# Performance work log

Measured on AMD Instinct MI355X. Metric: run time of the kernel, lower is better.

The kernel has to match this reference:

```python
import jax, jax.numpy as jnp
import numpy as np
import math

V, D, L, H, F, S_MAX = 32000, 512, 4, 8, 2048, 1024
DK = D // H
EPS = 1e-6


def _ln(x, g, b):
    # torch: gamma*(x-mean)/(std+eps)+beta with unbiased=False std, eps added to std
    mean = jnp.mean(x, axis=-1, keepdims=True)
    std = jnp.sqrt(jnp.mean((x - mean) ** 2, axis=-1, keepdims=True))
    return g * (x - mean) / (std + EPS) + b


def _pos_encoding(seq_len, d_model):
    pos = jnp.arange(seq_len, dtype=jnp.float32)[:, None]
    div = jnp.exp(jnp.arange(0, d_model, 2, dtype=jnp.float32) * (-math.log(10000.0) / d_model))
    pe = jnp.zeros((seq_len, d_model), dtype=jnp.float32)
    pe = pe.at[:, 0::2].set(jnp.sin(pos * div))
    pe = pe.at[:, 1::2].set(jnp.cos(pos * div))
    return pe


def setup_inputs() -> dict:
    key = jax.random.key(0)
    ks = jax.random.split(key, 20)
    n = lambda k, shape, s=0.02: (jax.random.normal(k, shape, dtype=jnp.float32) * s)
    inp = {
        "input_tokens": jax.random.randint(ks[0], (4, 1024), 0, V, dtype=jnp.int64),
        "tok_emb": n(ks[1], (V, D)),
        "gamma1": jnp.ones((L, D), jnp.float32), "beta1": jnp.zeros((L, D), jnp.float32),
        "wq": n(ks[2], (L, D, D)), "bq": jnp.zeros((L, D), jnp.float32),
        "wk": n(ks[3], (L, D, D)), "bk": jnp.zeros((L, D), jnp.float32),
        "wv": n(ks[4], (L, D, D)), "bv": jnp.zeros((L, D), jnp.float32),
        "wo": n(ks[5], (L, D, D)), "bo": jnp.zeros((L, D), jnp.float32),
        "gamma2": jnp.ones((L, D), jnp.float32), "beta2": jnp.zeros((L, D), jnp.float32),
        "w1": n(ks[6], (L, D, F)), "b1": jnp.zeros((L, F), jnp.float32),
        "w2": n(ks[7], (L, F, D)), "b2": jnp.zeros((L, D), jnp.float32),
        "gamma_f": jnp.ones((D,), jnp.float32), "beta_f": jnp.zeros((D,), jnp.float32),
        "w_out": n(ks[8], (D, V)), "b_out": jnp.zeros((V,), jnp.float32),
    }
    return inp


def reference(input_tokens, tok_emb, gamma1, beta1, wq, bq, wk, bk, wv, bv, wo, bo,
              gamma2, beta2, w1, b1, w2, b2, gamma_f, beta_f, w_out, b_out):
    B, S = input_tokens.shape
    # embedding * sqrt(d_model) + sinusoidal PE (dropout = identity in eval)
    x = tok_emb[input_tokens] * jnp.float32(math.sqrt(D)) + _pos_encoding(S, D)[None]
    causal = jnp.tril(jnp.ones((S, S), dtype=bool))[None, None]  # [1,1,S,S]
    scale = jnp.float32(1.0 / math.sqrt(DK))

    def block(x, p):
        g1, be1, Wq, Bq, Wk, Bk, Wv, Bv, Wo, Bo, g2, be2, W1, B1, W2, B2 = p
        h = _ln(x, g1, be1)
        q = (h @ Wq + Bq).reshape(B, S, H, DK).transpose(0, 2, 1, 3)
        k = (h @ Wk + Bk).reshape(B, S, H, DK).transpose(0, 2, 1, 3)
        v = (h @ Wv + Bv).reshape(B, S, H, DK).transpose(0, 2, 1, 3)
        scores = jnp.einsum('bhqd,bhkd->bhqk', q, k) * scale
        scores = jnp.where(causal, scores, jnp.float32(-1e9))  # masked_fill
        attn = jax.nn.softmax(scores, axis=-1)
        o = jnp.einsum('bhqk,bhkd->bhqd', attn, v)
        o = o.transpose(0, 2, 1, 3).reshape(B, S, D) @ Wo + Bo
        x = x + o
        h2 = _ln(x, g2, be2)
        ff = jax.nn.gelu(h2 @ W1 + B1, approximate=False) @ W2 + B2
        return x + ff, None

    params = (gamma1, beta1, wq, bq, wk, bk, wv, bv, wo, bo, gamma2, beta2, w1, b1, w2, b2)
    x, _ = jax.lax.scan(block, x, params)
    x = _ln(x, gamma_f, beta_f)
    logits = x @ w_out + b_out
    return logits
```

## Files before the change

### kernel.cpp

```cpp
#include <hip/hip_runtime.h>
#include <cstdint>
#include <cstddef>

typedef __attribute__((ext_vector_type(8))) short short8;
typedef __attribute__((ext_vector_type(4))) float f32x4;

#define DEV static __device__ __forceinline__

DEV short f2bf(float f) {
  unsigned u = __float_as_uint(f);
  u = (u + 0x7fffu + ((u >> 16) & 1u)) >> 16;
  return (short)u;
}

DEV void gload_lds16(const void* g, void* l) {
  __builtin_amdgcn_global_load_lds(
      (const __attribute__((address_space(1))) unsigned int*)(uintptr_t)g,
      (__attribute__((address_space(3))) unsigned int*)(uintptr_t)l,
      16, 0, 0);
}

DEV void transpose_tile32(const float* __restrict__ src, int sld,
                          short* __restrict__ dst, int dld,
                          int sr, int sc, int tid)
{
  __shared__ float tile[32][33];
  const int r = tid >> 5, c = tid & 31;
#pragma unroll
  for (int i = 0; i < 4; ++i)
    tile[r + 8 * i][c] = src[(size_t)(sr + r + 8 * i) * sld + sc + c];
  __syncthreads();
#pragma unroll
  for (int i = 0; i < 4; ++i)
    dst[(size_t)(sc + r + 8 * i) * dld + sr + c] = f2bf(tile[c][r + 8 * i]);
}

__global__ __launch_bounds__(256) void convert_all_k(
    const float* __restrict__ wq, const float* __restrict__ wk,
    const float* __restrict__ wv, const float* __restrict__ wo,
    const float* __restrict__ w1, const float* __restrict__ w2,
    const float* __restrict__ wout,
    const float* __restrict__ bq, const float* __restrict__ bk,
    const float* __restrict__ bv,
    short* __restrict__ wqkv_bt, short* __restrict__ wo_bt,
    short* __restrict__ w1_bt, short* __restrict__ w2_bt,
    short* __restrict__ wout_bt, float* __restrict__ bqkv)
{
  const int t = blockIdx.x, tid = threadIdx.x;
  if (t < 3072) {
    int layer = t / 768, rem = t % 768, mat = rem / 256, tt = rem % 256;
    int tr = tt / 16, tc = tt % 16;
    const float* src = (mat == 0 ? wq : mat == 1 ? wk : wv) + (size_t)layer * 262144;
    short* dst = wqkv_bt + (size_t)layer * 786432 + (size_t)mat * 262144;
    transpose_tile32(src, 512, dst, 512, tr * 32, tc * 32, tid);
  } else if (t < 4096) {
    int t2 = t - 3072;
    int layer = t2 / 256, tt = t2 % 256, tr = tt / 16, tc = tt % 16;
    transpose_tile32(wo + (size_t)layer * 262144, 512,
                     wo_bt + (size_t)layer * 262144, 512, tr * 32, tc * 32, tid);
  } else if (t < 8192) {
    int t2 = t - 4096;
    int layer = t2 / 1024, tt = t2 % 1024, tr = tt / 64, tc = tt % 64;
    transpose_tile32(w1 + (size_t)layer * 1048576, 2048,
                     w1_bt + (size_t)layer * 1048576, 512, tr * 32, tc * 32, tid);
  } else if (t < 12288) {
    int t2 = t - 8192;
    int layer = t2 / 1024, tt = t2 % 1024, tr = tt / 16, tc = tt % 16;
    transpose_tile32(w2 + (size_t)layer * 1048576, 512,
                     w2_bt + (size_t)layer * 1048576, 2048, tr * 32, tc * 32, tid);
  } else if (t < 28288) {
    int t2 = t - 12288;
    int tr = t2 / 1000, tc = t2 % 1000;
    transpose_tile32(wout, 32000, wout_bt, 512, tr * 32, tc * 32, tid);
  } else {
    int idx = (t - 28288) * 256 + tid;
    int layer = idx / 1536, j = idx % 1536;
    float v = (j < 512) ? bq[layer * 512 + j]
            : (j < 1024) ? bk[layer * 512 + j - 512]
                         : bv[layer * 512 + j - 1024];
    bqkv[idx] = v;
  }
}

__global__ __launch_bounds__(256) void embed_k(
    const int* __restrict__ tok, const float* __restrict__ emb, float* __restrict__ x)
{
  int idx = blockIdx.x * 256 + threadIdx.x;
  int d = idx & 511, bs = idx >> 9, s = bs & 1023;
  int t = tok[bs];
  float dv = expf((float)(d & ~1) * (-9.210340371976184f / 512.f));
  float ang = (float)s * dv;
  float pe = (d & 1) ? cosf(ang) : sinf(ang);
  x[idx] = emb[(size_t)t * 512 + d] * 22.62741699796952f + pe;
}

__global__ __launch_bounds__(256) void layernorm_k(
    const float* __restrict__ x, const float* __restrict__ g,
    const float* __restrict__ b, short* __restrict__ out)
{
  const int row = blockIdx.x, tid = threadIdx.x;
  const float* xr = x + (size_t)row * 512;
  float v0 = xr[tid], v1 = xr[tid + 256];
  float s = v0 + v1;
  __shared__ float rs[4], rq[4];
#pragma unroll
  for (int o = 32; o > 0; o >>= 1) s += __shfl_down(s, o, 64);
  if ((tid & 63) == 0) rs[tid >> 6] = s;
  __syncthreads();
  float mean = (rs[0] + rs[1] + rs[2] + rs[3]) * (1.f / 512.f);
  float d0 = v0 - mean, d1 = v1 - mean;
  float q = d0 * d0 + d1 * d1;
#pragma unroll
  for (int o = 32; o > 0; o >>= 1) q += __shfl_down(q, o, 64);
  if ((tid & 63) == 0) rq[tid >> 6] = q;
  __syncthreads();
  float var = (rq[0] + rq[1] + rq[2] + rq[3]) * (1.f / 512.f);
  float inv = 1.f / (sqrtf(var) + 1e-6f);
  out[(size_t)row * 512 + tid]       = f2bf(g[tid] * d0 * inv + b[tid]);
  out[(size_t)row * 512 + tid + 256] = f2bf(g[tid + 256] * d1 * inv + b[tid + 256]);
}

template<bool GELU, bool RES, bool OUTBF16>
__global__ __launch_bounds__(256) void gemm_bt(
    const short* __restrict__ A, const short* __restrict__ Bt,
    const float* __restrict__ bias, const float* __restrict__ resid,
    void* __restrict__ out, int M, int N, int K)
{
  __shared__ __align__(16) short lA[128 * 32];
  __shared__ __align__(16) short lB[128 * 32];
  const int tid = threadIdx.x;
  const int lane = tid & 63;
  const int w = tid >> 6, wr = w >> 1, wc = w & 1;
  const int lr = lane & 15, quad = lane >> 4;
  const int m0 = blockIdx.y * 128, n0 = blockIdx.x * 128;

  f32x4 acc[4][4] = {};

  const int c1 = tid, c2 = tid + 256;
  const short* Ab = A + (size_t)m0 * K;
  const short* Bb = Bt + (size_t)n0 * K;

  for (int k0 = 0; k0 < K; k0 += 32) {
    gload_lds16(Ab + (size_t)(c1 >> 2) * K + k0 + (c1 & 3) * 8, lA + c1 * 8);
    gload_lds16(Ab + (size_t)(c2 >> 2) * K + k0 + (c2 & 3) * 8, lA + c2 * 8);
    gload_lds16(Bb + (size_t)(c1 >> 2) * K + k0 + (c1 & 3) * 8, lB + c1 * 8);
    gload_lds16(Bb + (size_t)(c2 >> 2) * K + k0 + (c2 & 3) * 8, lB + c2 * 8);
    __syncthreads();
    short8 af[4], bf[4];
#pragma unroll
    for (int mi = 0; mi < 4; ++mi)
      af[mi] = *(const short8*)&lA[(wr * 64 + mi * 16 + lr) * 32 + quad * 8];
#pragma unroll
    for (int ni = 0; ni < 4; ++ni)
      bf[ni] = *(const short8*)&lB[(wc * 64 + ni * 16 + lr) * 32 + quad * 8];
#pragma unroll
    for (int mi = 0; mi < 4; ++mi)
#pragma unroll
      for (int ni = 0; ni < 4; ++ni)
        acc[mi][ni] = __builtin_amdgcn_mfma_f32_16x16x32_bf16(af[mi], bf[ni], acc[mi][ni], 0, 0, 0);
    __syncthreads();
  }

#pragma unroll
  for (int mi = 0; mi < 4; ++mi) {
#pragma unroll
    for (int ni = 0; ni < 4; ++ni) {
      const int n = n0 + wc * 64 + ni * 16 + lr;
      const float bn = bias[n];
#pragma unroll
      for (int r = 0; r < 4; ++r) {
        const int m = m0 + wr * 64 + mi * 16 + quad * 4 + r;
        float v = acc[mi][ni][r] + bn;
        if (GELU) v = 0.5f * v * (1.f + erff(v * 0.7071067811865475f));
        if (RES) v += resid[(size_t)m * N + n];
        if (OUTBF16) ((short*)out)[(size_t)m * N + n] = f2bf(v);
        else         ((float*)out)[(size_t)m * N + n] = v;
      }
    }
  }
}

__global__ __launch_bounds__(256) void attn_k(
    const short* __restrict__ qkv, short* __restrict__ attn_out)
{
  const int bh = blockIdx.y, b = bh >> 3, h = bh & 7;
  const int q0 = blockIdx.x * 64;
  const int tid = threadIdx.x, lane = tid & 63, w = tid >> 6;
  const int lr = lane & 15, quad = lane >> 4;
  const int RS = 1536;

  const short* qb = qkv + (size_t)b * 1024 * RS + h * 64;
  const short* kb = qb + 512;
  const short* vb = qb + 1024;

  __shared__ __align__(16) short lK[32 * 64];
  __shared__ __align__(16) short lVt[64 * 32];
  __shared__ __align__(16) short lP[4][16 * 32];

  const int qrow = q0 + w * 16 + lr;
  const short8 aq0 = *(const short8*)(qb + (size_t)qrow * RS + quad * 8);
  const short8 aq1 = *(const short8*)(qb + (size_t)qrow * RS + 32 + quad * 8);

  f32x4 o[4] = {};
  float mrow[4] = {-1e30f, -1e30f, -1e30f, -1e30f};
  float lrow[4] = {0.f, 0.f, 0.f, 0.f};

  const int kend = q0 + 64;
  for (int kt = 0; kt < kend; kt += 32) {
    {
      int r = tid >> 3, c = (tid & 7) * 8;
      gload_lds16(kb + (size_t)(kt + r) * RS + c, lK + r * 64 + c);
      short8 vv = *(const short8*)(vb + (size_t)(kt + r) * RS + c);
#pragma unroll
      for (int j = 0; j < 8; ++j) lVt[(c + j) * 32 + r] = vv[j];
    }
    __syncthreads();

    f32x4 st[2];
#pragma unroll
    for (int t = 0; t < 2; ++t) {
      const short8 bk0 = *(const short8*)&lK[(t * 16 + lr) * 64 + quad * 8];
      const short8 bk1 = *(const short8*)&lK[(t * 16 + lr) * 64 + 32 + quad * 8];
      f32x4 z = {0.f, 0.f, 0.f, 0.f};
      z = __builtin_amdgcn_mfma_f32_16x16x32_bf16(aq0, bk0, z, 0, 0, 0);
      z = __builtin_amdgcn_mfma_f32_16x16x32_bf16(aq1, bk1, z, 0, 0, 0);
      st[t] = z;
    }
    float sc[2][4];
#pragma unroll
    for (int t = 0; t < 2; ++t)
#pragma unroll
      for (int r = 0; r < 4; ++r) {
        int qg = q0 + w * 16 + quad * 4 + r;
        int kg = kt + t * 16 + lr;
        sc[t][r] = (kg <= qg) ? st[t][r] * 0.125f : -1e30f;
      }
#pragma unroll
    for (int r = 0; r < 4; ++r) {
      float tm = fmaxf(sc[0][r], sc[1][r]);
#pragma unroll
      for (int off = 1; off < 16; off <<= 1) tm = fmaxf(tm, __shfl_xor(tm, off, 64));
      float mnew = fmaxf(mrow[r], tm);
      float alpha = __expf(mrow[r] - mnew);
      mrow[r] = mnew;
      float p0 = __expf(sc[0][r] - mnew);
      float p1 = __expf(sc[1][r] - mnew);
      lP[w][(quad * 4 + r) * 32 + lr]      = f2bf(p0);
      lP[w][(quad * 4 + r) * 32 + 16 + lr] = f2bf(p1);
      float ps = p0 + p1;
#pragma unroll
      for (int off = 1; off < 16; off <<= 1) ps += __shfl_xor(ps, off, 64);
      lrow[r] = lrow[r] * alpha + ps;
#pragma unroll
      for (int ni = 0; ni < 4; ++ni) o[ni][r] *= alpha;
    }
    const short8 pa = *(const short8*)&lP[w][lr * 32 + quad * 8];
#pragma unroll
    for (int ni = 0; ni < 4; ++ni) {
      const short8 bv = *(const short8*)&lVt[(ni * 16 + lr) * 32 + quad * 8];
      o[ni] = __builtin_amdgcn_mfma_f32_16x16x32_bf16(pa, bv, o[ni], 0, 0, 0);
    }
    __syncthreads();
  }

#pragma unroll
  for (int ni = 0; ni < 4; ++ni)
#pragma unroll
    for (int r = 0; r < 4; ++r) {
      int qg = q0 + w * 16 + quad * 4 + r;
      float val = o[ni][r] / lrow[r];
      attn_out[((size_t)(b * 1024 + qg)) * 512 + h * 64 + ni * 16 + lr] = f2bf(val);
    }
}

extern "C" void kernel_launch(void* const* d_in, const int* in_sizes, int n_in,
                              void* d_out, int out_size, void* d_ws, size_t ws_size,
                              hipStream_t stream)
{
  (void)in_sizes; (void)n_in; (void)out_size; (void)ws_size;
  const int*   tokens  = (const int*)d_in[0];
  const float* tok_emb = (const float*)d_in[1];
  const float* gamma1  = (const float*)d_in[2];
  const float* beta1   = (const float*)d_in[3];
  const float* wq = (const float*)d_in[4];
  const float* bq = (const float*)d_in[5];
  const float* wk = (const float*)d_in[6];
  const float* bk = (const float*)d_in[7];
  const float* wv = (const float*)d_in[8];
  const float* bv = (const float*)d_in[9];
  const float* wo = (const float*)d_in[10];
  const float* bo = (const float*)d_in[11];
  const float* gamma2 = (const float*)d_in[12];
  const float* beta2  = (const float*)d_in[13];
  const float* w1 = (const float*)d_in[14];
  const float* b1 = (const float*)d_in[15];
  const float* w2 = (const float*)d_in[16];
  const float* b2 = (const float*)d_in[17];
  const float* gamma_f = (const float*)d_in[18];
  const float* beta_f  = (const float*)d_in[19];
  const float* w_out   = (const float*)d_in[20];
  const float* b_out   = (const float*)d_in[21];

  char* ws = (char*)d_ws;
  size_t off = 0;
  auto alloc = [&](size_t bytes) -> void* {
    void* p = ws + off; off += (bytes + 255) & ~(size_t)255; return p;
  };
  short* wqkv_bt = (short*)alloc(4ull * 1536 * 512 * 2);
  short* wo_bt   = (short*)alloc(4ull * 512 * 512 * 2);
  short* w1_bt   = (short*)alloc(4ull * 2048 * 512 * 2);
  short* w2_bt   = (short*)alloc(4ull * 512 * 2048 * 2);
  short* wout_bt = (short*)alloc(32000ull * 512 * 2);
  float* bqkv    = (float*)alloc(4ull * 1536 * 4);
  float* x       = (float*)alloc(4096ull * 512 * 4);
  short* hbuf    = (short*)alloc(4096ull * 512 * 2);
  short* qkv     = (short*)alloc(4096ull * 1536 * 2);
  short* attnout = (short*)alloc(4096ull * 512 * 2);
  short* ffn1    = (short*)alloc(4096ull * 2048 * 2);
  short* xf      = (short*)alloc(4096ull * 512 * 2);

  convert_all_k<<<28312, 256, 0, stream>>>(wq, wk, wv, wo, w1, w2, w_out, bq, bk, bv,
                                           wqkv_bt, wo_bt, w1_bt, w2_bt, wout_bt, bqkv);
  embed_k<<<8192, 256, 0, stream>>>(tokens, tok_emb, x);
  for (int l = 0; l < 4; ++l) {
    layernorm_k<<<4096, 256, 0, stream>>>(x, gamma1 + l * 512, beta1 + l * 512, hbuf);
    gemm_bt<false, false, true><<<dim3(12, 32), 256, 0, stream>>>(
        hbuf, wqkv_bt + (size_t)l * 786432, bqkv + l * 1536, nullptr, qkv, 4096, 1536, 512);
    attn_k<<<dim3(16, 32), 256, 0, stream>>>(qkv, attnout);
    gemm_bt<false, true, false><<<dim3(4, 32), 256, 0, stream>>>(
        attnout, wo_bt + (size_t)l * 262144, bo + l * 512, x, x, 4096, 512, 512);
    layernorm_k<<<4096, 256, 0, stream>>>(x, gamma2 + l * 512, beta2 + l * 512, hbuf);
    gemm_bt<true, false, true><<<dim3(16, 32), 256, 0, stream>>>(
        hbuf, w1_bt + (size_t)l * 1048576, b1 + l * 2048, nullptr, ffn1, 4096, 2048, 512);
    gemm_bt<false, true, false><<<dim3(4, 32), 256, 0, stream>>>(
        ffn1, w2_bt + (size_t)l * 1048576, b2 + l * 512, x, x, 4096, 512, 2048);
  }
  layernorm_k<<<4096, 256, 0, stream>>>(x, gamma_f, beta_f, xf);
  gemm_bt<false, false, false><<<dim3(250, 32), 256, 0, stream>>>(
      xf, wout_bt, b_out, nullptr, d_out, 4096, 32000, 512);
}
```

Before: 1.555 ms.

## Swizzle GEMM LDS layout and use 64-row tiles for N=512 GEMMs

Applies an XOR swizzle to the global-to-LDS source addressing and the matching fragment reads in the GEMM, to reduce LDS bank conflicts on the short8 loads. Adds a gemm64_bt variant with 64x128 tiles and uses it for the output-projection and FFN2 GEMMs (N=512). This doubles the grid from 128 to 256 blocks so more of the GPU's compute units are occupied. The smaller tiles lower per-block data reuse, and each wave computes a narrower 64x32 sub-tile.

Measured after the change: 1.504 ms. -3.3%, faster.

```diff
diff --git a/kernel.cpp b/kernel.cpp
--- a/kernel.cpp
+++ b/kernel.cpp
@@ -18,6 +18,11 @@
       (const __attribute__((address_space(1))) unsigned int*)(uintptr_t)g,
       (__attribute__((address_space(3))) unsigned int*)(uintptr_t)l,
       16, 0, 0);
+}
+
+DEV size_t swz_src(int c, int K, int k0) {
+  int r = c >> 2;
+  return (size_t)r * K + k0 + (size_t)(((c ^ r) & 3) << 3);
 }
 
 DEV void transpose_tile32(const float* __restrict__ src, int sld,
@@ -139,20 +144,21 @@
   const int c1 = tid, c2 = tid + 256;
   const short* Ab = A + (size_t)m0 * K;
   const short* Bb = Bt + (size_t)n0 * K;
+  const int sl = ((quad ^ lr) & 3) << 3;
 
   for (int k0 = 0; k0 < K; k0 += 32) {
-    gload_lds16(Ab + (size_t)(c1 >> 2) * K + k0 + (c1 & 3) * 8, lA + c1 * 8);
-    gload_lds16(Ab + (size_t)(c2 >> 2) * K + k0 + (c2 & 3) * 8, lA + c2 * 8);
-    gload_lds16(Bb + (size_t)(c1 >> 2) * K + k0 + (c1 & 3) * 8, lB + c1 * 8);
-    gload_lds16(Bb + (size_t)(c2 >> 2) * K + k0 + (c2 & 3) * 8, lB + c2 * 8);
+    gload_lds16(Ab + swz_src(c1, K, k0), lA + c1 * 8);
+    gload_lds16(Ab + swz_src(c2, K, k0), lA + c2 * 8);
+    gload_lds16(Bb + swz_src(c1, K, k0), lB + c1 * 8);
+    gload_lds16(Bb + swz_src(c2, K, k0), lB + c2 * 8);
     __syncthreads();
     short8 af[4], bf[4];
 #pragma unroll
     for (int mi = 0; mi < 4; ++mi)
-      af[mi] = *(const short8*)&lA[(wr * 64 + mi * 16 + lr) * 32 + quad * 8];
+      af[mi] = *(const short8*)&lA[(wr * 64 + mi * 16 + lr) * 32 + sl];
 #pragma unroll
     for (int ni = 0; ni < 4; ++ni)
-      bf[ni] = *(const short8*)&lB[(wc * 64 + ni * 16 + lr) * 32 + quad * 8];
+      bf[ni] = *(const short8*)&lB[(wc * 64 + ni * 16 + lr) * 32 + sl];
 #pragma unroll
     for (int mi = 0; mi < 4; ++mi)
 #pragma unroll
@@ -170,6 +176,66 @@
 #pragma unroll
       for (int r = 0; r < 4; ++r) {
         const int m = m0 + wr * 64 + mi * 16 + quad * 4 + r;
+        float v = acc[mi][ni][r] + bn;
+        if (GELU) v = 0.5f * v * (1.f + erff(v * 0.7071067811865475f));
+        if (RES) v += resid[(size_t)m * N + n];
+        if (OUTBF16) ((short*)out)[(size_t)m * N + n] = f2bf(v);
+        else         ((float*)out)[(size_t)m * N + n] = v;
+      }
+    }
+  }
+}
+
+template<bool GELU, bool RES, bool OUTBF16>
+__global__ __launch_bounds__(256) void gemm64_bt(
+    const short* __restrict__ A, const short* __restrict__ Bt,
+    const float* __restrict__ bias, const float* __restrict__ resid,
+    void* __restrict__ out, int M, int N, int K)
+{
+  __shared__ __align__(16) short lA[64 * 32];
+  __shared__ __align__(16) short lB[128 * 32];
+  const int tid = threadIdx.x;
+  const int lane = tid & 63;
+  const int w = tid >> 6;
+  const int lr = lane & 15, quad = lane >> 4;
+  const int m0 = blockIdx.y * 64, n0 = blockIdx.x * 128;
+
+  f32x4 acc[4][2] = {};
+
+  const int c2 = tid + 256;
+  const short* Ab = A + (size_t)m0 * K;
+  const short* Bb = Bt + (size_t)n0 * K;
+  const int sl = ((quad ^ lr) & 3) << 3;
+
+  for (int k0 = 0; k0 < K; k0 += 32) {
+    gload_lds16(Ab + swz_src(tid, K, k0), lA + tid * 8);
+    gload_lds16(Bb + swz_src(tid, K, k0), lB + tid * 8);
+    gload_lds16(Bb + swz_src(c2,  K, k0), lB + c2 * 8);
+    __syncthreads();
+    short8 af[4], bf[2];
+#pragma unroll
+    for (int mi = 0; mi < 4; ++mi)
+      af[mi] = *(const short8*)&lA[(mi * 16 + lr) * 32 + sl];
+#pragma unroll
+    for (int ni = 0; ni < 2; ++ni)
+      bf[ni] = *(const short8*)&lB[(w * 32 + ni * 16 + lr) * 32 + sl];
+#pragma unroll
+    for (int mi = 0; mi < 4; ++mi)
+#pragma unroll
+      for (int ni = 0; ni < 2; ++ni)
+        acc[mi][ni] = __builtin_amdgcn_mfma_f32_16x16x32_bf16(af[mi], bf[ni], acc[mi][ni], 0, 0, 0);
+    __syncthreads();
+  }
+
+#pragma unroll
+  for (int mi = 0; mi < 4; ++mi) {
+#pragma unroll
+    for (int ni = 0; ni < 2; ++ni) {
+      const int n = n0 + w * 32 + ni * 16 + lr;
+      const float bn = bias[n];
+#pragma unroll
+      for (int r = 0; r < 4; ++r) {
+        const int m = m0 + mi * 16 + quad * 4 + r;
         float v = acc[mi][ni][r] + bn;
         if (GELU) v = 0.5f * v * (1.f + erff(v * 0.7071067811865475f));
         if (RES) v += resid[(size_t)m * N + n];
@@ -327,12 +393,12 @@
     gemm_bt<false, false, true><<<dim3(12, 32), 256, 0, stream>>>(
         hbuf, wqkv_bt + (size_t)l * 786432, bqkv + l * 1536, nullptr, qkv, 4096, 1536, 512);
     attn_k<<<dim3(16, 32), 256, 0, stream>>>(qkv, attnout);
-    gemm_bt<false, true, false><<<dim3(4, 32), 256, 0, stream>>>(
+    gemm64_bt<false, true, false><<<dim3(4, 64), 256, 0, stream>>>(
         attnout, wo_bt + (size_t)l * 262144, bo + l * 512, x, x, 4096, 512, 512);
     layernorm_k<<<4096, 256, 0, stream>>>(x, gamma2 + l * 512, beta2 + l * 512, hbuf);
     gemm_bt<true, false, true><<<dim3(16, 32), 256, 0, stream>>>(
         hbuf, w1_bt + (size_t)l * 1048576, b1 + l * 2048, nullptr, ffn1, 4096, 2048, 512);
-    gemm_bt<false, true, false><<<dim3(4, 32), 256, 0, stream>>>(
+    gemm64_bt<false, true, false><<<dim3(4, 64), 256, 0, stream>>>(
         ffn1, w2_bt + (size_t)l * 1048576, b2 + l * 512, x, x, 4096, 512, 2048);
   }
   layernorm_k<<<4096, 256, 0, stream>>>(x, gamma_f, beta_f, xf);
```
